# Optimization experiments

Measured on AMD Instinct MI355X. Metric: run time of the kernel, lower is better.

The kernel has to match this reference:

```python
import jax, jax.numpy as jnp
import numpy as np


def _gcn_conv(x, W, b, src, dst, deg_inv_sqrt, n_nodes):
    # x: [N, Fin], W: [Fin, Fout]; edges (with self-loops): src, dst [E+N]
    h = x @ W  # [N, Fout]
    norm = deg_inv_sqrt[src] * deg_inv_sqrt[dst]  # [E+N]
    msgs = h[src] * norm[:, None]  # gather-multiply
    out = jax.ops.segment_sum(msgs, dst, num_segments=n_nodes)  # scatter-add
    return out + b


def setup_inputs() -> dict:
    key = jax.random.key(0)
    k1, k2, k3, k4 = jax.random.split(key, 4)
    N, E, FIN, HID, OUT = 100000, 3200000, 128, 32, 32
    x = jax.random.normal(k1, (N, FIN), dtype=jnp.float32)
    edge_index = jax.random.randint(k2, (2, E), 0, N, dtype=jnp.int64)
    W1 = jax.random.normal(k3, (FIN, HID), dtype=jnp.float32) * (1.0 / np.sqrt(FIN))
    b1 = jnp.zeros((HID,), dtype=jnp.float32)
    W2 = jax.random.normal(k4, (HID, OUT), dtype=jnp.float32) * (1.0 / np.sqrt(HID))
    b2 = jnp.zeros((OUT,), dtype=jnp.float32)
    return {"x": x, "edge_index": edge_index, "W1": W1, "b1": b1, "W2": W2, "b2": b2}


def reference(x, edge_index, W1, b1, W2, b2):
    n = x.shape[0]
    # GCNConv defaults: add self-loops, symmetric normalization D^-1/2 (A+I) D^-1/2
    loops = jnp.arange(n, dtype=edge_index.dtype)
    src = jnp.concatenate([edge_index[0], loops])
    dst = jnp.concatenate([edge_index[1], loops])
    deg = jax.ops.segment_sum(jnp.ones_like(dst, dtype=x.dtype), dst, num_segments=n)
    deg_inv_sqrt = jnp.where(deg > 0, jax.lax.rsqrt(jnp.maximum(deg, 1.0)), 0.0)
    h = jax.nn.relu(_gcn_conv(x, W1, b1, src, dst, deg_inv_sqrt, n))  # hidden layer + ReLU
    out = jax.nn.relu(_gcn_conv(h, W2, b2, src, dst, deg_inv_sqrt, n))  # last layer + last_activation relu
    return out
```

## Files before the change

### kernel.cpp

```cpp
#include <hip/hip_runtime.h>
#include <hip/hip_fp16.h>

#define FIN 128
#define HID 32
#define BSHIFT 8
#define BNODES 256
#define CHUNK 2048
#define NBMAX 512
#define CAPB 8960
#define G1ROWS 64
#define XPAD 4


__global__ __launch_bounds__(256) void chunk_sort_kernel(const int* __restrict__ src,
                                                         const int* __restrict__ dst,
                                                         int* __restrict__ ec,
                                                         unsigned short* __restrict__ offt,
                                                         int E, int nb) {
    __shared__ int hist[NBMAX];
    __shared__ int pref[NBMAX];
    __shared__ int wsum[128];
    __shared__ int sorted[CHUNK];
    int c = blockIdx.x, t = threadIdx.x;
    int beg = c * CHUNK;
    int cnt = min(CHUNK, E - beg);
    for (int i = t; i < nb; i += 256) hist[i] = 0;
    __syncthreads();
    int bk[8], ent[8];
    #pragma unroll
    for (int j = 0; j < 8; ++j) {
        int i = t + j * 256;
        if (i < cnt) {
            int d = dst[beg + i];
            bk[j]  = ((unsigned)d) >> BSHIFT;
            ent[j] = src[beg + i] | ((d & (BNODES - 1)) << 24);
            atomicAdd(&hist[bk[j]], 1);
        } else bk[j] = -1;
    }
    __syncthreads();
    if (t < 128) {
        int s = 0;
        #pragma unroll
        for (int j = 0; j < 4; ++j) {
            int idx = t * 4 + j;
            int v = (idx < nb) ? hist[idx] : 0;
            pref[idx] = s; s += v;
        }
        wsum[t] = s;
    }
    __syncthreads();
    if (t == 0) { int run = 0; for (int j = 0; j < 128; ++j) { int v = wsum[j]; wsum[j] = run; run += v; } }
    __syncthreads();
    for (int i = t; i < nb; i += 256) { int p = pref[i] + wsum[i >> 2]; pref[i] = p; hist[i] = p; }
    __syncthreads();
    #pragma unroll
    for (int j = 0; j < 8; ++j) {
        if (bk[j] >= 0) {
            int p = atomicAdd(&hist[bk[j]], 1);
            sorted[p] = ent[j];
        }
    }
    __syncthreads();
    for (int i = t; i < cnt; i += 256) ec[(size_t)c * CHUNK + i] = sorted[i];
    unsigned short* row = offt + (size_t)c * (nb + 1);
    for (int i = t; i < nb; i += 256) row[i] = (unsigned short)pref[i];
    if (t == 0) row[nb] = (unsigned short)cnt;
}


__global__ __launch_bounds__(1024) void bucket_build_kernel(const int* __restrict__ ec,
                                                            const unsigned short* __restrict__ offt,
                                                            int* __restrict__ entries,
                                                            float* __restrict__ dinv,
                                                            int* __restrict__ rowbeg,
                                                            int* __restrict__ rowcnt,
                                                            int n, int nb, int nchunks, int cap) {
    __shared__ int raw[CAPB];
    __shared__ int srt[CAPB];
    __shared__ int hist[BNODES];
    __shared__ int pref[BNODES];
    __shared__ int cursor[BNODES];
    __shared__ int wsum[64];
    __shared__ int nfill;
    int b = blockIdx.x, t = threadIdx.x;
    if (t < BNODES) hist[t] = 0;
    if (t == 0) nfill = 0;
    __syncthreads();
    for (int c = t; c < nchunks; c += 1024) {
        const unsigned short* row = offt + (size_t)c * (nb + 1);
        int s = row[b], e2 = row[b + 1];
        int m = e2 - s;
        if (m > 0) {
            int base = atomicAdd(&nfill, m);
            const int* p = ec + (size_t)c * CHUNK + s;
            for (int k = 0; k < m; ++k) {
                int e = p[k];
                if (base + k < CAPB) raw[base + k] = e;
                atomicAdd(&hist[((unsigned)e) >> 24], 1);
            }
        }
    }
    __syncthreads();
    int total = min(nfill, CAPB);
    if (t < 64) {
        int s = 0;
        #pragma unroll
        for (int j = 0; j < 4; ++j) { int v = hist[t * 4 + j]; pref[t * 4 + j] = s; s += v; }
        wsum[t] = s;
    }
    __syncthreads();
    if (t == 0) { int run = 0; for (int j = 0; j < 64; ++j) { int v = wsum[j]; wsum[j] = run; run += v; } }
    __syncthreads();
    if (t < BNODES) { int p = pref[t] + wsum[t >> 2]; pref[t] = p; cursor[t] = p; }
    __syncthreads();
    for (int i = t; i < total; i += 1024) {
        int e = raw[i];
        int p = atomicAdd(&cursor[((unsigned)e) >> 24], 1);
        srt[p] = e;
    }
    __syncthreads();
    int* ep = entries + (size_t)b * cap;
    for (int i = t; i < total; i += 1024) ep[i] = srt[i];
    int node = b * BNODES + t;
    if (t < BNODES && node < n) {
        int deg = hist[t];
        dinv[node]   = rsqrtf((float)deg + 1.0f);
        rowbeg[node] = b * cap + pref[t];
        rowcnt[node] = deg;
    }
}


__global__ __launch_bounds__(256) void gemm1_kernel(const float* __restrict__ x,
                                                    const float* __restrict__ W,
                                                    const float* __restrict__ dinv,
                                                    __half* __restrict__ h16, int n) {
    __shared__ float Ws[FIN * HID];
    __shared__ float xs[G1ROWS][FIN + XPAD];
    int t = threadIdx.x;
    for (int i = t; i < FIN * HID; i += 256) Ws[i] = W[i];
    int row0 = blockIdx.x * G1ROWS;
    for (int idx = t; idx < G1ROWS * (FIN / 4); idx += 256) {
        int r  = idx >> 5;
        int c4 = (idx & 31) * 4;
        int row = row0 + r;
        float4 v = (row < n) ? *(const float4*)&x[(size_t)row * FIN + c4]
                             : make_float4(0.f, 0.f, 0.f, 0.f);
        *(float4*)&xs[r][c4] = v;
    }
    __syncthreads();
    int tr = t >> 3, tc = t & 7;
    int r0 = tr * 2, c0 = tc * 4;
    float4 a0 = make_float4(0.f, 0.f, 0.f, 0.f);
    float4 a1 = make_float4(0.f, 0.f, 0.f, 0.f);
    #pragma unroll 8
    for (int k4 = 0; k4 < FIN / 4; ++k4) {
        float4 xv0 = *(const float4*)&xs[r0][k4 * 4];
        float4 xv1 = *(const float4*)&xs[r0 + 1][k4 * 4];
        float4 w0 = *(const float4*)&Ws[(k4 * 4 + 0) * HID + c0];
        float4 w1 = *(const float4*)&Ws[(k4 * 4 + 1) * HID + c0];
        float4 w2 = *(const float4*)&Ws[(k4 * 4 + 2) * HID + c0];
        float4 w3 = *(const float4*)&Ws[(k4 * 4 + 3) * HID + c0];
        a0.x = fmaf(xv0.x, w0.x, a0.x); a0.y = fmaf(xv0.x, w0.y, a0.y);
        a0.z = fmaf(xv0.x, w0.z, a0.z); a0.w = fmaf(xv0.x, w0.w, a0.w);
        a0.x = fmaf(xv0.y, w1.x, a0.x); a0.y = fmaf(xv0.y, w1.y, a0.y);
        a0.z = fmaf(xv0.y, w1.z, a0.z); a0.w = fmaf(xv0.y, w1.w, a0.w);
        a0.x = fmaf(xv0.z, w2.x, a0.x); a0.y = fmaf(xv0.z, w2.y, a0.y);
        a0.z = fmaf(xv0.z, w2.z, a0.z); a0.w = fmaf(xv0.z, w2.w, a0.w);
        a0.x = fmaf(xv0.w, w3.x, a0.x); a0.y = fmaf(xv0.w, w3.y, a0.y);
        a0.z = fmaf(xv0.w, w3.z, a0.z); a0.w = fmaf(xv0.w, w3.w, a0.w);
        a1.x = fmaf(xv1.x, w0.x, a1.x); a1.y = fmaf(xv1.x, w0.y, a1.y);
        a1.z = fmaf(xv1.x, w0.z, a1.z); a1.w = fmaf(xv1.x, w0.w, a1.w);
        a1.x = fmaf(xv1.y, w1.x, a1.x); a1.y = fmaf(xv1.y, w1.y, a1.y);
        a1.z = fmaf(xv1.y, w1.z, a1.z); a1.w = fmaf(xv1.y, w1.w, a1.w);
        a1.x = fmaf(xv1.z, w2.x, a1.x); a1.y = fmaf(xv1.z, w2.y, a1.y);
        a1.z = fmaf(xv1.z, w2.z, a1.z); a1.w = fmaf(xv1.z, w2.w, a1.w);
        a1.x = fmaf(xv1.w, w3.x, a1.x); a1.y = fmaf(xv1.w, w3.y, a1.y);
        a1.z = fmaf(xv1.w, w3.z, a1.z); a1.w = fmaf(xv1.w, w3.w, a1.w);
    }
    #pragma unroll
    for (int rr = 0; rr < 2; ++rr) {
        int row = row0 + r0 + rr;
        float4 a = rr ? a1 : a0;
        float di = (row < n) ? dinv[row] : 0.f;
        float sc = (row < n) ? di : 0.f;
        __half2 p0 = __floats2half2_rn(a.x * sc, a.y * sc);
        __half2 p1 = __floats2half2_rn(a.z * sc, a.w * sc);
        __half2* dst = (__half2*)&h16[(size_t)row * HID + c0];
        dst[0] = p0;
        dst[1] = p1;
    }
}


__global__ __launch_bounds__(256) void gather_kernel(const int* __restrict__ entries,
                                                     const int* __restrict__ rowbeg,
                                                     const int* __restrict__ rowcnt,
                                                     const float* __restrict__ dinv,
                                                     const __half* __restrict__ h16,
                                                     const float* __restrict__ bias,
                                                     float* __restrict__ out, int n, int sent) {
    int g = threadIdx.x >> 5, f = threadIdx.x & 31;
    int i = blockIdx.x * 8 + g;
    if (i >= n) return;
    float di = dinv[i];
    float s = __half2float(h16[(size_t)i * HID + f]);
    int beg = rowbeg[i], cnt = rowcnt[i];
    for (int base = 0; base < cnt; base += 32) {
        int idx = beg + base + f;
        int sv = ((base + f) < cnt) ? entries[idx] : sent;
        float hv[32];
        #pragma unroll
        for (int j = 0; j < 32; ++j) {
            int e = __shfl(sv, j, 32);
            hv[j] = __half2float(h16[(size_t)(e & 0xFFFFFF) * HID + f]);
        }
        #pragma unroll
        for (int j = 0; j < 32; ++j) s += hv[j];
    }
    float r = bias[f] + di * s;
    out[(size_t)i * HID + f] = fmaxf(r, 0.f);
}


__global__ __launch_bounds__(256) void gemm2_kernel(const float* __restrict__ hin,
                                                    const float* __restrict__ W,
                                                    const float* __restrict__ dinv,
                                                    __half* __restrict__ h16, int n) {
    __shared__ float Ws[HID * HID];
    __shared__ float hs[8][HID];
    int t = threadIdx.x;
    for (int i = t; i < HID * HID; i += 256) Ws[i] = W[i];
    int row0 = blockIdx.x * 8;
    {
        int r = t >> 5, c = t & 31;
        int row = row0 + r;
        hs[r][c] = (row < n) ? hin[(size_t)row * HID + c] : 0.f;
    }
    __syncthreads();
    int r = t >> 5, col = t & 31;
    int row = row0 + r;
    if (row < n) {
        float s = 0.f;
        #pragma unroll
        for (int k = 0; k < HID; ++k) s += hs[r][k] * Ws[k * HID + col];
        h16[(size_t)row * HID + col] = __float2half(s * dinv[row]);
    } else {
        h16[(size_t)row * HID + col] = __float2half(0.f);
    }
}

extern "C" void kernel_launch(void* const* d_in, const int* in_sizes, int n_in,
                              void* d_out, int out_size, void* d_ws, size_t ws_size,
                              hipStream_t stream) {
    const float* x  = (const float*)d_in[0];
    const int*   ei = (const int*)d_in[1];
    const float* W1 = (const float*)d_in[2];
    const float* b1 = (const float*)d_in[3];
    const float* W2 = (const float*)d_in[4];
    const float* b2 = (const float*)d_in[5];
    float* out = (float*)d_out;

    int n = in_sizes[0] / FIN;
    int E = in_sizes[1] / 2;
    const int* src = ei;
    const int* dst = ei + E;

    int nb = (n + BNODES - 1) / BNODES;
    int nchunks = (E + CHUNK - 1) / CHUNK;
    int g1grid = (n + G1ROWS) / G1ROWS;
    int npad = g1grid * G1ROWS;
    int cap = CAPB;

    char* ws = (char*)d_ws;
    size_t off = 0;
    auto alloc = [&](size_t bytes) { char* p = ws + off; off += (bytes + 255) & ~(size_t)255; return p; };
    int*            ec      = (int*)alloc((size_t)nchunks * CHUNK * 4);
    unsigned short* offt    = (unsigned short*)alloc((size_t)nchunks * (nb + 1) * 2);
    int*            entries = (int*)alloc((size_t)nb * cap * 4);
    float*          dinv    = (float*)alloc((size_t)n * 4);
    int*            rowbeg  = (int*)alloc((size_t)n * 4);
    int*            rowcnt  = (int*)alloc((size_t)n * 4);
    float*          acc     = (float*)alloc((size_t)n * HID * 4);
    __half*         hh      = (__half*)alloc((size_t)npad * HID * 2);

    chunk_sort_kernel<<<nchunks, 256, 0, stream>>>(src, dst, ec, offt, E, nb);
    bucket_build_kernel<<<nb, 1024, 0, stream>>>(ec, offt, entries, dinv, rowbeg, rowcnt,
                                                 n, nb, nchunks, cap);

    gemm1_kernel<<<g1grid, 256, 0, stream>>>(x, W1, dinv, hh, n);
    gather_kernel<<<(n + 7) / 8, 256, 0, stream>>>(entries, rowbeg, rowcnt, dinv, hh, b1, acc, n, n);

    gemm2_kernel<<<(n + 8) / 8, 256, 0, stream>>>(acc, W2, dinv, hh, n);
    gather_kernel<<<(n + 7) / 8, 256, 0, stream>>>(entries, rowbeg, rowcnt, dinv, hh, b2, out, n, n);
}
```

Baseline: 267.3 us.

## Use 4 threads per node with 16-byte gathers and tile gemm2 like gemm1

The gather kernel now gives each destination node 4 threads instead of a 32-lane group. Each thread loads 8 half features with one 16-byte load per neighbor, four neighbors at a time, and writes its outputs as float4. This aims to replace many 2-byte per-lane gathers and shuffles with fewer, wider memory requests and more nodes per block. gemm2 is restructured into a 64-row register-tiled float4 kernel modeled on gemm1, giving more reuse per block. The trade-off is less parallelism within high-degree nodes, since each node's edge list is walked serially in steps of 4.

```diff
diff --git a/kernel.cpp b/kernel.cpp
--- a/kernel.cpp
+++ b/kernel.cpp
@@ -182,8 +182,7 @@
     for (int rr = 0; rr < 2; ++rr) {
         int row = row0 + r0 + rr;
         float4 a = rr ? a1 : a0;
-        float di = (row < n) ? dinv[row] : 0.f;
-        float sc = (row < n) ? di : 0.f;
+        float sc = (row < n) ? dinv[row] : 0.f;
         __half2 p0 = __floats2half2_rn(a.x * sc, a.y * sc);
         __half2 p1 = __floats2half2_rn(a.z * sc, a.w * sc);
         __half2* dst = (__half2*)&h16[(size_t)row * HID + c0];
@@ -200,26 +199,51 @@
                                                      const __half* __restrict__ h16,
                                                      const float* __restrict__ bias,
                                                      float* __restrict__ out, int n, int sent) {
-    int g = threadIdx.x >> 5, f = threadIdx.x & 31;
-    int i = blockIdx.x * 8 + g;
+    int t = threadIdx.x;
+    int g = t >> 2, q = t & 3;
+    int i = blockIdx.x * 64 + g;
     if (i >= n) return;
     float di = dinv[i];
-    float s = __half2float(h16[(size_t)i * HID + f]);
+    float s0, s1, s2, s3, s4, s5, s6, s7;
+    {
+        float4 raw = *(const float4*)&h16[(size_t)i * HID + q * 8];
+        __half2 h0 = *(__half2*)&raw.x, h1 = *(__half2*)&raw.y;
+        __half2 h2 = *(__half2*)&raw.z, h3 = *(__half2*)&raw.w;
+        float2 f0 = __half22float2(h0), f1 = __half22float2(h1);
+        float2 f2 = __half22float2(h2), f3 = __half22float2(h3);
+        s0 = f0.x; s1 = f0.y; s2 = f1.x; s3 = f1.y;
+        s4 = f2.x; s5 = f2.y; s6 = f3.x; s7 = f3.y;
+    }
     int beg = rowbeg[i], cnt = rowcnt[i];
-    for (int base = 0; base < cnt; base += 32) {
-        int idx = beg + base + f;
-        int sv = ((base + f) < cnt) ? entries[idx] : sent;
-        float hv[32];
-        #pragma unroll
-        for (int j = 0; j < 32; ++j) {
-            int e = __shfl(sv, j, 32);
-            hv[j] = __half2float(h16[(size_t)(e & 0xFFFFFF) * HID + f]);
+    for (int base = 0; base < cnt; base += 4) {
+        int e[4];
+        #pragma unroll
+        for (int u = 0; u < 4; ++u)
+            e[u] = (base + u < cnt) ? (entries[beg + base + u] & 0xFFFFFF) : sent;
+        float4 raw[4];
+        #pragma unroll
+        for (int u = 0; u < 4; ++u)
+            raw[u] = *(const float4*)&h16[(size_t)e[u] * HID + q * 8];
+        #pragma unroll
+        for (int u = 0; u < 4; ++u) {
+            __half2 h0 = *(__half2*)&raw[u].x, h1 = *(__half2*)&raw[u].y;
+            __half2 h2 = *(__half2*)&raw[u].z, h3 = *(__half2*)&raw[u].w;
+            float2 f0 = __half22float2(h0), f1 = __half22float2(h1);
+            float2 f2 = __half22float2(h2), f3 = __half22float2(h3);
+            s0 += f0.x; s1 += f0.y; s2 += f1.x; s3 += f1.y;
+            s4 += f2.x; s5 += f2.y; s6 += f3.x; s7 += f3.y;
         }
-        #pragma unroll
-        for (int j = 0; j < 32; ++j) s += hv[j];
-    }
-    float r = bias[f] + di * s;
-    out[(size_t)i * HID + f] = fmaxf(r, 0.f);
+    }
+    float4 b0 = *(const float4*)&bias[q * 8];
+    float4 b1 = *(const float4*)&bias[q * 8 + 4];
+    float4 o0, o1;
+    o0.x = fmaxf(b0.x + di * s0, 0.f); o0.y = fmaxf(b0.y + di * s1, 0.f);
+    o0.z = fmaxf(b0.z + di * s2, 0.f); o0.w = fmaxf(b0.w + di * s3, 0.f);
+    o1.x = fmaxf(b1.x + di * s4, 0.f); o1.y = fmaxf(b1.y + di * s5, 0.f);
+    o1.z = fmaxf(b1.z + di * s6, 0.f); o1.w = fmaxf(b1.w + di * s7, 0.f);
+    float* op = &out[(size_t)i * HID + q * 8];
+    *(float4*)op = o0;
+    *(float4*)(op + 4) = o1;
 }
 
 
@@ -228,25 +252,58 @@
                                                     const float* __restrict__ dinv,
                                                     __half* __restrict__ h16, int n) {
     __shared__ float Ws[HID * HID];
-    __shared__ float hs[8][HID];
+    __shared__ float hs[G1ROWS][HID + XPAD];
     int t = threadIdx.x;
     for (int i = t; i < HID * HID; i += 256) Ws[i] = W[i];
-    int row0 = blockIdx.x * 8;
-    {
-        int r = t >> 5, c = t & 31;
+    int row0 = blockIdx.x * G1ROWS;
+    for (int idx = t; idx < G1ROWS * (HID / 4); idx += 256) {
+        int r  = idx >> 3;
+        int c4 = (idx & 7) * 4;
         int row = row0 + r;
-        hs[r][c] = (row < n) ? hin[(size_t)row * HID + c] : 0.f;
-    }
-    __syncthreads();
-    int r = t >> 5, col = t & 31;
-    int row = row0 + r;
-    if (row < n) {
-        float s = 0.f;
-        #pragma unroll
-        for (int k = 0; k < HID; ++k) s += hs[r][k] * Ws[k * HID + col];
-        h16[(size_t)row * HID + col] = __float2half(s * dinv[row]);
-    } else {
-        h16[(size_t)row * HID + col] = __float2half(0.f);
+        float4 v = (row < n) ? *(const float4*)&hin[(size_t)row * HID + c4]
+                             : make_float4(0.f, 0.f, 0.f, 0.f);
+        *(float4*)&hs[r][c4] = v;
+    }
+    __syncthreads();
+    int tr = t >> 3, tc = t & 7;
+    int r0 = tr * 2, c0 = tc * 4;
+    float4 a0 = make_float4(0.f, 0.f, 0.f, 0.f);
+    float4 a1 = make_float4(0.f, 0.f, 0.f, 0.f);
+    #pragma unroll
+    for (int k4 = 0; k4 < HID / 4; ++k4) {
+        float4 xv0 = *(const float4*)&hs[r0][k4 * 4];
+        float4 xv1 = *(const float4*)&hs[r0 + 1][k4 * 4];
+        float4 w0 = *(const float4*)&Ws[(k4 * 4 + 0) * HID + c0];
+        float4 w1 = *(const float4*)&Ws[(k4 * 4 + 1) * HID + c0];
+        float4 w2 = *(const float4*)&Ws[(k4 * 4 + 2) * HID + c0];
+        float4 w3 = *(const float4*)&Ws[(k4 * 4 + 3) * HID + c0];
+        a0.x = fmaf(xv0.x, w0.x, a0.x); a0.y = fmaf(xv0.x, w0.y, a0.y);
+        a0.z = fmaf(xv0.x, w0.z, a0.z); a0.w = fmaf(xv0.x, w0.w, a0.w);
+        a0.x = fmaf(xv0.y, w1.x, a0.x); a0.y = fmaf(xv0.y, w1.y, a0.y);
+        a0.z = fmaf(xv0.y, w1.z, a0.z); a0.w = fmaf(xv0.y, w1.w, a0.w);
+        a0.x = fmaf(xv0.z, w2.x, a0.x); a0.y = fmaf(xv0.z, w2.y, a0.y);
+        a0.z = fmaf(xv0.z, w2.z, a0.z); a0.w = fmaf(xv0.z, w2.w, a0.w);
+        a0.x = fmaf(xv0.w, w3.x, a0.x); a0.y = fmaf(xv0.w, w3.y, a0.y);
+        a0.z = fmaf(xv0.w, w3.z, a0.z); a0.w = fmaf(xv0.w, w3.w, a0.w);
+        a1.x = fmaf(xv1.x, w0.x, a1.x); a1.y = fmaf(xv1.x, w0.y, a1.y);
+        a1.z = fmaf(xv1.x, w0.z, a1.z); a1.w = fmaf(xv1.x, w0.w, a1.w);
+        a1.x = fmaf(xv1.y, w1.x, a1.x); a1.y = fmaf(xv1.y, w1.y, a1.y);
+        a1.z = fmaf(xv1.y, w1.z, a1.z); a1.w = fmaf(xv1.y, w1.w, a1.w);
+        a1.x = fmaf(xv1.z, w2.x, a1.x); a1.y = fmaf(xv1.z, w2.y, a1.y);
+        a1.z = fmaf(xv1.z, w2.z, a1.z); a1.w = fmaf(xv1.z, w2.w, a1.w);
+        a1.x = fmaf(xv1.w, w3.x, a1.x); a1.y = fmaf(xv1.w, w3.y, a1.y);
+        a1.z = fmaf(xv1.w, w3.z, a1.z); a1.w = fmaf(xv1.w, w3.w, a1.w);
+    }
+    #pragma unroll
+    for (int rr = 0; rr < 2; ++rr) {
+        int row = row0 + r0 + rr;
+        float4 a = rr ? a1 : a0;
+        float sc = (row < n) ? dinv[row] : 0.f;
+        __half2 p0 = __floats2half2_rn(a.x * sc, a.y * sc);
+        __half2 p1 = __floats2half2_rn(a.z * sc, a.w * sc);
+        __half2* dst = (__half2*)&h16[(size_t)row * HID + c0];
+        dst[0] = p0;
+        dst[1] = p1;
     }
 }
 
@@ -268,8 +325,8 @@
 
     int nb = (n + BNODES - 1) / BNODES;
     int nchunks = (E + CHUNK - 1) / CHUNK;
-    int g1grid = (n + G1ROWS) / G1ROWS;
-    int npad = g1grid * G1ROWS;
+    int ggrid = (n + G1ROWS) / G1ROWS;
+    int npad = ggrid * G1ROWS;
     int cap = CAPB;
 
     char* ws = (char*)d_ws;
@@ -288,9 +345,9 @@
     bucket_build_kernel<<<nb, 1024, 0, stream>>>(ec, offt, entries, dinv, rowbeg, rowcnt,
                                                  n, nb, nchunks, cap);
 
-    gemm1_kernel<<<g1grid, 256, 0, stream>>>(x, W1, dinv, hh, n);
-    gather_kernel<<<(n + 7) / 8, 256, 0, stream>>>(entries, rowbeg, rowcnt, dinv, hh, b1, acc, n, n);
-
-    gemm2_kernel<<<(n + 8) / 8, 256, 0, stream>>>(acc, W2, dinv, hh, n);
-    gather_kernel<<<(n + 7) / 8, 256, 0, stream>>>(entries, rowbeg, rowcnt, dinv, hh, b2, out, n, n);
-}
+    gemm1_kernel<<<ggrid, 256, 0, stream>>>(x, W1, dinv, hh, n);
+    gather_kernel<<<(n + 63) / 64, 256, 0, stream>>>(entries, rowbeg, rowcnt, dinv, hh, b1, acc, n, n);
+
+    gemm2_kernel<<<ggrid, 256, 0, stream>>>(acc, W2, dinv, hh, n);
+    gather_kernel<<<(n + 63) / 64, 256, 0, stream>>>(entries, rowbeg, rowcnt, dinv, hh, b2, out, n, n);
+}
```

New measurement: 292.1 us. 9.3% more time.
